# Kernel optimization log

Hardware: AMD Instinct MI355X
Metric: run time of the kernel (lower is better)

The kernel has to match this reference:

```python
import jax, jax.numpy as jnp
import numpy as np

B, S, V, D, H, KVH, L = 2, 1024, 8192, 1024, 16, 4, 8
HD = D // H          # 64, head dim
KV = KVH * HD        # 256, kv projection width
HID = 2736           # max(16, ceil(2*4*1024/48)*16)
NS = 4               # num_skip_weights = min(L//2, L - L//2)
SOFTCAP = 30.0
ROPE_BASE = 10000.0
RS_INIT = 1.0 / np.sqrt(L)


def setup_inputs() -> dict:
    key = jax.random.key(0)
    ks = iter(jax.random.split(key, 64))
    def rn(shape, s=0.02):
        return jax.random.normal(next(ks), shape, dtype=jnp.float32) * s
    inp = {}
    inp['idx'] = jax.random.randint(next(ks), (B, S), 0, V)
    inp['tok_emb'] = rn((V, D))
    inp['embed_norm_w'] = 1.0 + rn((D,))
    inp['resid_mix'] = jnp.stack([1.0 + rn((L, D), 0.05), rn((L, D), 0.05)], axis=1)  # [L,2,D]
    inp['attn_norm_w'] = 1.0 + rn((L, D))
    inp['mlp_norm_w'] = 1.0 + rn((L, D))
    inp['attn_scale'] = RS_INIT + rn((L, D))
    inp['mlp_scale'] = RS_INIT + rn((L, D))
    inp['Wq'] = rn((L, D, D))
    inp['Wk'] = rn((L, KV, D))
    inp['Wv'] = rn((L, KV, D))
    conv = lambda C: rn((L, 3, C), 0.1).at[:, 2, :].add(1.0)  # curr ~ 1, prev ~ 0
    inp['q_conv_w'] = conv(D)
    inp['k_conv_w'] = conv(KV)
    inp['v_conv_w'] = conv(KV)
    inp['q_gain'] = jnp.eye(H, dtype=jnp.float32)[None] + rn((L, H, H))
    inp['post_attn_norm_w'] = 1.0 + rn((L, D))
    inp['Wo'] = rn((L, D, D))
    inp['Wfc'] = rn((L, HID, D))
    inp['Wgate'] = rn((L, HID, D))
    inp['h_conv_w'] = rn((L, 3, HID), 0.1).at[:, 2, :].add(1.0)
    inp['h_norm_w'] = 1.0 + rn((L, HID))
    inp['Wmproj'] = rn((L, D, HID))
    inp['skip_weights'] = RS_INIT + rn((NS, D))
    inp['skip_gates'] = rn((NS, D), 0.1)
    inp['final_norm_w'] = 1.0 + rn((D,))
    inp['lm_head_w'] = rn((V, D))
    inp['bigram_head'] = rn((V, V))
    inp['bigram_scale'] = 0.02 + rn((V,), 0.005)
    inp['bigram_gate'] = rn((D,), 0.1)
    inp['unigram_bias'] = rn((V,), 0.01)
    return inp


def _rmsnorm(x, w=None):
    eps = jnp.finfo(x.dtype).eps
    y = x * jax.lax.rsqrt(jnp.mean(x * x, axis=-1, keepdims=True) + eps)
    return y * w if w is not None else y


def _dwconv(x, w):  # x [B,S,C], w [3,C]: causal depthwise 3-tap conv
    n = x.shape[1]
    xp = jnp.pad(x, ((0, 0), (2, 0), (0, 0)))
    return w[0] * xp[:, :n] + w[1] * xp[:, 1:n + 1] + w[2] * xp[:, 2:]


def _rope_tables(seqlen):
    inv_freq = 1.0 / (ROPE_BASE ** (jnp.arange(0, HD, 2, dtype=jnp.float32) / HD))
    freqs = jnp.outer(jnp.arange(seqlen, dtype=jnp.float32), inv_freq)  # [S, HD//2]
    return jnp.cos(freqs)[None, None], jnp.sin(freqs)[None, None]


def _apply_rope(x, cos, sin):
    half = x.shape[-1] // 2
    x1, x2 = x[..., :half], x[..., half:]
    return jnp.concatenate([x1 * cos + x2 * sin, -x1 * sin + x2 * cos], axis=-1)


def reference(idx, tok_emb, embed_norm_w, resid_mix, attn_norm_w, mlp_norm_w, attn_scale, mlp_scale, Wq, Wk, Wv, q_conv_w, k_conv_w, v_conv_w, q_gain, post_attn_norm_w, Wo, Wfc, Wgate, h_conv_w, h_norm_w, Wmproj, skip_weights, skip_gates, final_norm_w, lm_head_w, bigram_head, bigram_scale, bigram_gate, unigram_bias):
    cos, sin = _rope_tables(S)
    causal = jnp.tril(jnp.ones((S, S), dtype=bool))

    def attn(x, i):
        q = _dwconv(x @ Wq[i].T, q_conv_w[i]).reshape(B, S, H, HD).transpose(0, 2, 1, 3)
        k = _dwconv(x @ Wk[i].T, k_conv_w[i]).reshape(B, S, KVH, HD).transpose(0, 2, 1, 3)
        v = _dwconv(x @ Wv[i].T, v_conv_w[i]).reshape(B, S, KVH, HD).transpose(0, 2, 1, 3)
        q = _apply_rope(_rmsnorm(q), cos, sin)
        k = _apply_rope(_rmsnorm(k), cos, sin)
        q = jnp.einsum('hg,bgsd->bhsd', q_gain[i], q)
        kr = jnp.repeat(k, H // KVH, axis=1)
        vr = jnp.repeat(v, H // KVH, axis=1)
        scores = jnp.einsum('bhsd,bhtd->bhst', q, kr) / np.sqrt(HD).astype(np.float32)
        scores = jnp.where(causal, scores, -jnp.inf)
        p = jax.nn.softmax(scores, axis=-1)
        y = jnp.einsum('bhst,bhtd->bhsd', p, vr).transpose(0, 2, 1, 3).reshape(B, S, D)
        return _rmsnorm(y, post_attn_norm_w[i]) @ Wo[i].T

    def mlp(x, i):
        h = (x @ Wfc[i].T) * jax.nn.silu(x @ Wgate[i].T)
        h = _rmsnorm(_dwconv(h, h_conv_w[i]), h_norm_w[i])
        return h @ Wmproj[i].T

    def block(x, x0, i):
        x = resid_mix[i, 0] * x + resid_mix[i, 1] * x0
        x = x + attn_scale[i] * attn(_rmsnorm(x, attn_norm_w[i]), i)
        x = x + mlp_scale[i] * mlp(_rmsnorm(x, mlp_norm_w[i]), i)
        return x

    x = _rmsnorm(tok_emb[idx], embed_norm_w)
    x0 = x
    enc = L // 2
    skips = []
    for i in range(enc):
        x = block(x, x0, i)
        skips.append(x)
    for j in range(L - enc):
        if j < NS:
            x = x + (skip_weights[j] * jax.nn.sigmoid(skip_gates[j]))[None, None, :] * skips.pop()
        x = block(x, x0, enc + j)
    x = _rmsnorm(x, final_norm_w)

    logits = x @ lm_head_w.T + unigram_bias
    gate = jax.nn.sigmoid(x @ bigram_gate)[..., None]        # [B,S,1]
    logits = logits + gate * (bigram_head[idx] * bigram_scale)
    return SOFTCAP * jnp.tanh(logits / SOFTCAP)
```

## Files before the change

### kernel.cpp

```cpp
#include <hip/hip_runtime.h>
#include <hip/hip_bf16.h>
#include <cstdint>
#include <cstddef>

#define B_   2
#define S_   1024
#define V_   8192
#define D_   1024
#define H_   16
#define KVH_ 4
#define L_   8
#define HD_  64
#define KV_  256
#define HID_ 2736
#define HIDP 2752
#define NT_  (B_*S_)
#define EPSF 1.1920928955078125e-7f
#define SOFTCAPF 30.0f

typedef __bf16 bf8 __attribute__((ext_vector_type(8)));
typedef __bf16 bf4 __attribute__((ext_vector_type(4)));
typedef float  f4  __attribute__((ext_vector_type(4)));

#define GLDS16(g, l) __builtin_amdgcn_global_load_lds( \
    (const __attribute__((address_space(1))) void*)(g), \
    (__attribute__((address_space(3))) void*)(l), 16, 0, 0)

__device__ __forceinline__ float wsum(float v){
#pragma unroll
  for (int m = 32; m >= 1; m >>= 1) v += __shfl_xor(v, m, 64);
  return v;
}
__device__ __forceinline__ float blocksum256(float v){
  __shared__ float red[4];
  v = wsum(v);
  if ((threadIdx.x & 63) == 0) red[threadIdx.x >> 6] = v;
  __syncthreads();
  return red[0] + red[1] + red[2] + red[3];
}
__device__ __forceinline__ float4 ld4b(const __bf16* p, size_t i4){
  bf4 v = ((const bf4*)p)[i4];
  return make_float4((float)v[0], (float)v[1], (float)v[2], (float)v[3]);
}

template<int BM, int BN, int OUT>
__global__ __launch_bounds__(256) void k_gemm(
    const __bf16* __restrict__ A, const __bf16* __restrict__ Wt,
    void* __restrict__ Cv, int M, int N, int K, int lda, int mtiles)
{
  constexpr int SMEM = (BM + BN) * 128;
  __shared__ __attribute__((aligned(16))) unsigned char smem[SMEM];
  __bf16* As = (__bf16*)smem;
  __bf16* Bs = (__bf16*)(smem + BM*128);

  const int tid  = threadIdx.x;
  const int nwg = gridDim.x;
  const int wg  = (blockIdx.x & 7) * (nwg >> 3) + (blockIdx.x >> 3);
  const int bm   = wg % mtiles;
  const int bn   = wg / mtiles;
  const int m0   = bm * BM, n0 = bn * BN;
  const int lane = tid & 63, wv = tid >> 6;
  const int wm   = (wv >> 1) * (BM / 2);
  const int wn   = (wv & 1) * (BN / 2);
  const int fr   = lane & 15, g = lane >> 4;
  constexpr int MI = BM / 32;
  constexpr int NJ = BN / 32;
  constexpr int AP = BM / 32;
  constexpr int BP = BN / 32;

  f4 acc[MI][NJ] = {};

  const int rs = lane >> 3, ss = lane & 7;
  const int cseg = ss ^ ((wv*8 + rs) & 7);
  const __bf16* aq[AP];
#pragma unroll
  for (int p = 0; p < AP; ++p)
    aq[p] = A + (size_t)(m0 + wv*8 + p*32 + rs) * lda + cseg*8;
  const __bf16* bq[BP];
#pragma unroll
  for (int p = 0; p < BP; ++p) {
    int rB = n0 + wv*8 + p*32 + rs; if (rB > N-1) rB = N-1;
    bq[p] = Wt + (size_t)rB * K + cseg*8;
  }

  for (int k0 = 0; k0 < K; k0 += 64) {
    __syncthreads();
#pragma unroll
    for (int p = 0; p < AP; ++p) GLDS16(aq[p] + k0, As + (wv*8 + p*32)*64);
#pragma unroll
    for (int p = 0; p < BP; ++p) GLDS16(bq[p] + k0, Bs + (wv*8 + p*32)*64);
    __syncthreads();

#pragma unroll
    for (int ks = 0; ks < 2; ++ks) {
      const int sgo = (((ks*4 + g) ^ (fr & 7)) << 3);
      bf8 af[MI], bf[NJ];
#pragma unroll
      for (int i = 0; i < MI; ++i)
        af[i] = *(const bf8*)&As[(wm + i*16 + fr)*64 + sgo];
#pragma unroll
      for (int j = 0; j < NJ; ++j)
        bf[j] = *(const bf8*)&Bs[(wn + j*16 + fr)*64 + sgo];
#pragma unroll
      for (int i = 0; i < MI; ++i)
#pragma unroll
        for (int j = 0; j < NJ; ++j)
          acc[i][j] = __builtin_amdgcn_mfma_f32_16x16x32_bf16(af[i], bf[j], acc[i][j], 0, 0, 0);
    }
  }

  const int rbase = g << 2;
#pragma unroll
  for (int i = 0; i < MI; ++i) {
    int gm = m0 + wm + i*16 + rbase;
#pragma unroll
    for (int j = 0; j < NJ; ++j) {
      int gn = n0 + wn + j*16 + fr;
      if (gn < N) {
        if constexpr (OUT == 1) {
#pragma unroll
          for (int r = 0; r < 4; ++r)
            ((__bf16*)Cv)[(size_t)(gm + r) * N + gn] = (__bf16)acc[i][j][r];
        } else {
#pragma unroll
          for (int r = 0; r < 4; ++r)
            ((float*)Cv)[(size_t)(gm + r) * N + gn] = acc[i][j][r];
        }
      }
    }
  }
}

#define STG8(t, h, b) do { \
    if ((h) < 2) { \
      const __bf16* _s = A + (size_t)(m0 + (h)*128 + w16 + rsub) * lda + (t)*32 + sseg*8; \
      GLDS16(_s, smem + (b)*32768 + ((h)*128 + w16) * 64); \
    } else { \
      int _rB = n0 + ((h)-2)*128 + w16 + rsub; if (_rB > N-1) _rB = N-1; \
      const __bf16* _s = Wt + (size_t)_rB * K + (t)*32 + sseg*8; \
      GLDS16(_s, smem + (b)*32768 + 16384 + (((h)-2)*128 + w16) * 64); \
    } } while (0)

#define LDA8(b, r, gg) (*(const bf8*)(smem + (b)*32768 + (r)*64 + (((gg) ^ ((((r)>>3)&1)<<1)))*16))
#define LDB8(b, r, gg) (*(const bf8*)(smem + (b)*32768 + 16384 + (r)*64 + (((gg) ^ ((((r)>>3)&1)<<1)))*16))

#define PH8(bt, q, dostage, st, sh, sb, W) do { \
    const int _r0 = wr*128 + ((q)>>1)*64 + fr; \
    const int _c0 = wc*64 + ((q)&1)*32 + fr; \
    bf8 _a0 = LDA8(bt, _r0 +  0, g); \
    bf8 _a1 = LDA8(bt, _r0 + 16, g); \
    bf8 _a2 = LDA8(bt, _r0 + 32, g); \
    bf8 _a3 = LDA8(bt, _r0 + 48, g); \
    bf8 _b0 = LDB8(bt, _c0 +  0, g); \
    bf8 _b1 = LDB8(bt, _c0 + 16, g); \
    if (dostage) STG8(st, sh, sb); \
    if ((W) == 4)      asm volatile("s_waitcnt vmcnt(4)" ::: "memory"); \
    else if ((W) == 0) asm volatile("s_waitcnt vmcnt(0)" ::: "memory"); \
    asm volatile("" ::: "memory"); \
    __builtin_amdgcn_s_barrier(); \
    asm volatile("" ::: "memory"); \
    __builtin_amdgcn_s_setprio(1); \
    acc[((q)>>1)*4+0][((q)&1)*2+0] = __builtin_amdgcn_mfma_f32_16x16x32_bf16(_a0, _b0, acc[((q)>>1)*4+0][((q)&1)*2+0], 0,0,0); \
    acc[((q)>>1)*4+0][((q)&1)*2+1] = __builtin_amdgcn_mfma_f32_16x16x32_bf16(_a0, _b1, acc[((q)>>1)*4+0][((q)&1)*2+1], 0,0,0); \
    acc[((q)>>1)*4+1][((q)&1)*2+0] = __builtin_amdgcn_mfma_f32_16x16x32_bf16(_a1, _b0, acc[((q)>>1)*4+1][((q)&1)*2+0], 0,0,0); \
    acc[((q)>>1)*4+1][((q)&1)*2+1] = __builtin_amdgcn_mfma_f32_16x16x32_bf16(_a1, _b1, acc[((q)>>1)*4+1][((q)&1)*2+1], 0,0,0); \
    acc[((q)>>1)*4+2][((q)&1)*2+0] = __builtin_amdgcn_mfma_f32_16x16x32_bf16(_a2, _b0, acc[((q)>>1)*4+2][((q)&1)*2+0], 0,0,0); \
    acc[((q)>>1)*4+2][((q)&1)*2+1] = __builtin_amdgcn_mfma_f32_16x16x32_bf16(_a2, _b1, acc[((q)>>1)*4+2][((q)&1)*2+1], 0,0,0); \
    acc[((q)>>1)*4+3][((q)&1)*2+0] = __builtin_amdgcn_mfma_f32_16x16x32_bf16(_a3, _b0, acc[((q)>>1)*4+3][((q)&1)*2+0], 0,0,0); \
    acc[((q)>>1)*4+3][((q)&1)*2+1] = __builtin_amdgcn_mfma_f32_16x16x32_bf16(_a3, _b1, acc[((q)>>1)*4+3][((q)&1)*2+1], 0,0,0); \
    __builtin_amdgcn_s_setprio(0); \
    asm volatile("" ::: "memory"); \
    __builtin_amdgcn_s_barrier(); \
    asm volatile("" ::: "memory"); \
  } while (0)

template<int OUT>
__global__ __launch_bounds__(512, 2) void k_gemm8(
    const __bf16* __restrict__ A, const __bf16* __restrict__ Wt,
    void* __restrict__ Cv, int M, int N, int K, int lda, int mtiles,
    const int* __restrict__ idx, const float* __restrict__ gateb,
    const float* __restrict__ bhd, const float* __restrict__ bsc,
    const float* __restrict__ ub)
{
  __shared__ __attribute__((aligned(16))) unsigned char smem[98304];
  const int tid = threadIdx.x;
  const int nwg = gridDim.x;
  const int wg  = (blockIdx.x & 7) * (nwg >> 3) + (blockIdx.x >> 3);
  const int bm = wg % mtiles, bnn = wg / mtiles;
  const int m0 = bm << 8, n0 = bnn << 8;
  const int l = tid & 63, wid = tid >> 6;
  const int wr = wid >> 2, wc = wid & 3;
  const int fr = l & 15, g = l >> 4;

  f4 acc[8][4] = {};

  const int w16  = wid * 16;
  const int rsub = l >> 2;
  const int sseg = (l & 3) ^ ((l >= 32) ? 2 : 0);

  const int nk = K >> 5;
  const int ni = nk >> 1;

  STG8(0, 0, 0); STG8(0, 1, 0); STG8(0, 2, 0); STG8(0, 3, 0);
  STG8(1, 0, 1); STG8(1, 1, 1); STG8(1, 2, 1); STG8(1, 3, 1);
  asm volatile("s_waitcnt vmcnt(4)" ::: "memory");
  asm volatile("" ::: "memory");
  __builtin_amdgcn_s_barrier();
  asm volatile("" ::: "memory");

  int b0 = 0;
  for (int i = 0; i < ni; ++i) {
    const int b1 = (b0 == 2) ? 0 : b0 + 1;
    const int b2 = (b1 == 2) ? 0 : b1 + 1;
    const bool nlast = (i + 1 < ni);
    const int t2 = 2*i + 2, t3 = 2*i + 3;
    PH8(b0, 0, nlast, t2, 0, b2, -1);
    PH8(b0, 1, nlast, t2, 1, b2, -1);
    PH8(b0, 2, nlast, t2, 2, b2, -1);
    PH8(b0, 3, nlast, t2, 3, b2, nlast ? 4 : 0);
    PH8(b1, 0, nlast, t3, 0, b0, -1);
    PH8(b1, 1, nlast, t3, 1, b0, -1);
    PH8(b1, 2, nlast, t3, 2, b0, -1);
    PH8(b1, 3, nlast, t3, 3, b0, nlast ? 4 : -1);
    b0 = b2;
  }

  if constexpr (OUT == 1) {
    __bf16* C = (__bf16*)Cv;
#pragma unroll
    for (int ii = 0; ii < 8; ++ii) {
      int gm = m0 + wr*128 + ii*16 + g*4;
#pragma unroll
      for (int j = 0; j < 4; ++j) {
        int gn = n0 + wc*64 + j*16 + fr;
        if (gn < N) {
#pragma unroll
          for (int r = 0; r < 4; ++r)
            C[(size_t)(gm + r) * N + gn] = (__bf16)acc[ii][j][r];
        }
      }
    }
  } else {
    float* EP = (float*)smem;
    __syncthreads();
#pragma unroll
    for (int pass = 0; pass < 4; ++pass) {
      if (wr == (pass >> 1)) {
#pragma unroll
        for (int a = 0; a < 4; ++a) {
          int ii = (pass & 1)*4 + a;
#pragma unroll
          for (int j = 0; j < 4; ++j)
#pragma unroll
            for (int r = 0; r < 4; ++r)
              EP[(a*16 + g*4 + r)*256 + wc*64 + j*16 + fr] = acc[ii][j][r];
        }
      }
      __syncthreads();
#pragma unroll
      for (int it = 0; it < 8; ++it) {
        int row = it*8 + (tid >> 6);
        int c0  = (tid & 63) << 2;
        int grow = m0 + pass*64 + row;
        int gn = n0 + c0;
        float gt = gateb[grow];
        int tk = idx[grow];
        float4 a4 = *(float4*)&EP[row*256 + c0];
        float4 b4 = *(const float4*)&bhd[(size_t)tk * V_ + gn];
        float4 u4 = *(const float4*)&ub[gn];
        float4 s4 = *(const float4*)&bsc[gn];
        float4 o;
        o.x = SOFTCAPF * tanhf((a4.x + u4.x + gt*b4.x*s4.x) / SOFTCAPF);
        o.y = SOFTCAPF * tanhf((a4.y + u4.y + gt*b4.y*s4.y) / SOFTCAPF);
        o.z = SOFTCAPF * tanhf((a4.z + u4.z + gt*b4.z*s4.z) / SOFTCAPF);
        o.w = SOFTCAPF * tanhf((a4.w + u4.w + gt*b4.w*s4.w) / SOFTCAPF);
        *(float4*)&((float*)Cv)[(size_t)grow * N + gn] = o;
      }
      __syncthreads();
    }
  }
}
#undef PH8
#undef LDA8
#undef LDB8
#undef STG8

__global__ void k_cvt(const float* __restrict__ s, __bf16* __restrict__ d,
                      int perL, int K, int Kpad, long dstL, long dstOff, long nd4)
{
  long i = (long)blockIdx.x * 256 + threadIdx.x;
  if (i >= nd4) return;
  const int kp4 = Kpad >> 2;
  long row = i / kp4;
  int  c   = (int)(i % kp4) << 2;
  long layer = row / perL, r = row % perL;
  bf4 o;
  if (c < K) {
    float4 v = *(const float4*)(s + (layer*perL + r) * (long)K + c);
    o[0] = (__bf16)v.x; o[1] = (__bf16)v.y; o[2] = (__bf16)v.z; o[3] = (__bf16)v.w;
  } else { o[0] = o[1] = o[2] = o[3] = (__bf16)0.f; }
  *(bf4*)(d + layer*dstL + dstOff + (long)r*Kpad + c) = o;
}

__global__ void k_embed(const int* __restrict__ idx, const float* __restrict__ emb,
                        const float* __restrict__ wn, float* __restrict__ x, float* __restrict__ x0)
{
  const int r = blockIdx.x, t = threadIdx.x;
  const float4 v = ((const float4*)(emb + (size_t)idx[r] * D_))[t];
  float ss = blocksum256(v.x*v.x + v.y*v.y + v.z*v.z + v.w*v.w);
  float rs = rsqrtf(ss / (float)D_ + EPSF);
  const float4 w = ((const float4*)wn)[t];
  float4 o = make_float4(v.x*rs*w.x, v.y*rs*w.y, v.z*rs*w.z, v.w*rs*w.w);
  ((float4*)(x  + (size_t)r * D_))[t] = o;
  ((float4*)(x0 + (size_t)r * D_))[t] = o;
}

__global__ void k_blockstart(
    float* __restrict__ x, const float* __restrict__ x0,
    const __bf16* __restrict__ t1, const float* __restrict__ msc,
    float* __restrict__ skstore, const float* __restrict__ skread, int same,
    const float* __restrict__ skw, const float* __restrict__ skg,
    const float* __restrict__ mix, const float* __restrict__ nw,
    __bf16* __restrict__ xn)
{
  const int r = blockIdx.x, t = threadIdx.x;
  const size_t i4 = (size_t)r * 256 + t;
  float4 xv = ((float4*)x)[i4];
  if (t1) {
    float4 tv = ld4b(t1, i4);
    float4 s  = ((const float4*)msc)[t];
    xv.x += s.x*tv.x; xv.y += s.y*tv.y; xv.z += s.z*tv.z; xv.w += s.w*tv.w;
  }
  if (skstore) ((float4*)skstore)[i4] = xv;
  if (skw) {
    float4 sv;
    if (same) sv = xv;
    else      sv = ((const float4*)skread)[i4];
    float4 w = ((const float4*)skw)[t];
    float4 g = ((const float4*)skg)[t];
    xv.x += w.x / (1.f + __expf(-g.x)) * sv.x;
    xv.y += w.y / (1.f + __expf(-g.y)) * sv.y;
    xv.z += w.z / (1.f + __expf(-g.z)) * sv.z;
    xv.w += w.w / (1.f + __expf(-g.w)) * sv.w;
  }
  float4 x0v = ((const float4*)x0)[i4];
  float4 m0  = ((const float4*)mix)[t];
  float4 m1  = ((const float4*)(mix + D_))[t];
  float4 nv;
  nv.x = m0.x*xv.x + m1.x*x0v.x; nv.y = m0.y*xv.y + m1.y*x0v.y;
  nv.z = m0.z*xv.z + m1.z*x0v.z; nv.w = m0.w*xv.w + m1.w*x0v.w;
  ((float4*)x)[i4] = nv;
  float ss = blocksum256(nv.x*nv.x + nv.y*nv.y + nv.z*nv.z + nv.w*nv.w);
  float rs = rsqrtf(ss / (float)D_ + EPSF);
  const float4 w = ((const float4*)nw)[t];
  bf4 o = { (__bf16)(nv.x*rs*w.x), (__bf16)(nv.y*rs*w.y),
            (__bf16)(nv.z*rs*w.z), (__bf16)(nv.w*rs*w.w) };
  ((bf4*)xn)[i4] = o;
}

__global__ void k_addnorm(float* __restrict__ x, const __bf16* __restrict__ t1,
                          const float* __restrict__ sc, const float* __restrict__ nw,
                          __bf16* __restrict__ xn,
                          const float* __restrict__ bg, float* __restrict__ gateb)
{
  const int r = blockIdx.x, t = threadIdx.x;
  const size_t i4 = (size_t)r * 256 + t;
  float4 xv = ((float4*)x)[i4];
  float4 tv = ld4b(t1, i4);
  float4 s  = ((const float4*)sc)[t];
  xv.x += s.x*tv.x; xv.y += s.y*tv.y; xv.z += s.z*tv.z; xv.w += s.w*tv.w;
  ((float4*)x)[i4] = xv;
  float ss = blocksum256(xv.x*xv.x + xv.y*xv.y + xv.z*xv.z + xv.w*xv.w);
  float rs = rsqrtf(ss / (float)D_ + EPSF);
  const float4 w = ((const float4*)nw)[t];
  float ox = xv.x*rs*w.x, oy = xv.y*rs*w.y, oz = xv.z*rs*w.z, ow = xv.w*rs*w.w;
  bf4 o = { (__bf16)ox, (__bf16)oy, (__bf16)oz, (__bf16)ow };
  ((bf4*)xn)[i4] = o;
  if (bg) {
    float4 b4 = ((const float4*)bg)[t];
    float gd = ox*b4.x + oy*b4.y + oz*b4.z + ow*b4.w;
    __syncthreads();
    float gs = blocksum256(gd);
    if (t == 0) gateb[r] = 1.f / (1.f + __expf(-gs));
  }
}

__global__ void k_rmsnormb(const float* __restrict__ in, const float* __restrict__ w,
                           __bf16* __restrict__ out)
{
  const int r = blockIdx.x, t = threadIdx.x;
  float4 v = ((const float4*)(in + (size_t)r * D_))[t];
  float ss = blocksum256(v.x*v.x + v.y*v.y + v.z*v.z + v.w*v.w);
  float rs = rsqrtf(ss / (float)D_ + EPSF);
  const float4 w4 = ((const float4*)w)[t];
  bf4 o = { (__bf16)(v.x*rs*w4.x), (__bf16)(v.y*rs*w4.y),
            (__bf16)(v.z*rs*w4.z), (__bf16)(v.w*rs*w4.w) };
  ((bf4*)(out + (size_t)r * D_))[t] = o;
}

__device__ __forceinline__ float conv3b(const __bf16* buf, int tok, int s, int ld, int col,
                                        const float* w, int C, int c){
  const __bf16* p0 = buf + (size_t)tok * ld + col;
  float a  = (s >= 2) ? (float)p0[-2*ld] : 0.f;
  float bb = (s >= 1) ? (float)p0[-ld]   : 0.f;
  return w[c]*a + w[C + c]*bb + w[2*C + c]*(float)p0[0];
}

__global__ __launch_bounds__(256) void k_prep(
    const __bf16* __restrict__ qkv,
    const float* __restrict__ qcw, const float* __restrict__ kcw, const float* __restrict__ vcw,
    const float* __restrict__ qgain,
    __bf16* __restrict__ q2, __bf16* __restrict__ k2, __bf16* __restrict__ v2)
{
  const int tok = blockIdx.x;
  const int s = tok & (S_ - 1);
  const int t = threadIdx.x, lane = t & 63, w = t >> 6;
  __shared__ float qsh[1024];

  const int j = lane & 31;
  float freq = __expf(-(float)j * (9.210340371976184f / 32.f));
  float sn, cs;
  __sincosf((float)s * freq, &sn, &cs);

#pragma unroll
  for (int k = 0; k < 4; ++k) {
    int c = t + k*256;
    float qc = conv3b(qkv, tok, s, 1536, c, qcw, D_, c);
    float ssq = wsum(qc * qc);
    float qn = qc * rsqrtf(ssq / 64.f + EPSF);
    float pr = __shfl_xor(qn, 32, 64);
    qsh[c] = qn * cs + ((lane < 32) ? pr * sn : -pr * sn);
  }
  __syncthreads();
  float qg[16];
#pragma unroll
  for (int g = 0; g < 16; ++g) qg[g] = qsh[g*64 + lane];
#pragma unroll
  for (int k = 0; k < 4; ++k) {
    int h = (k << 2) + w;
    float acc = 0.f;
#pragma unroll
    for (int g = 0; g < 16; ++g) acc += qgain[h*16 + g] * qg[g];
    q2[(size_t)tok * D_ + h*64 + lane] = (__bf16)acc;
  }

  {
    float kc = conv3b(qkv, tok, s, 1536, 1024 + t, kcw, KV_, t);
    float ssk = wsum(kc * kc);
    float kn = kc * rsqrtf(ssk / 64.f + EPSF);
    float pk = __shfl_xor(kn, 32, 64);
    k2[(size_t)tok * KV_ + t] = (__bf16)(kn * cs + ((lane < 32) ? pk * sn : -pk * sn));
  }
  v2[(size_t)tok * KV_ + t] = (__bf16)conv3b(qkv, tok, s, 1536, 1280 + t, vcw, KV_, t);
}

#define LDK 72
__global__ __launch_bounds__(256) void k_attn(
    const __bf16* __restrict__ q2, const __bf16* __restrict__ k2,
    const __bf16* __restrict__ v2, float* __restrict__ y)
{
  __shared__ __attribute__((aligned(16))) __bf16 Ks[64*LDK];
  __shared__ __attribute__((aligned(16))) __bf16 Vt[64*LDK];
  __shared__ __attribute__((aligned(16))) __bf16 Ps[4][16*LDK];

  const int id = blockIdx.x;
  const int h  = (id >> 4) & 15;
  const int b  = id >> 8;
  const int qb = b ? (15 - (id & 15)) : (id & 15);
  const int tid = threadIdx.x, l = tid & 63, wq = tid >> 6;
  const int g = l >> 4, fr = l & 15;
  const int kvh = h >> 2;
  const int qrow = qb*64 + wq*16 + fr;

  bf8 qf[2];
#pragma unroll
  for (int ks = 0; ks < 2; ++ks)
    qf[ks] = *(const bf8*)&q2[(size_t)(b*S_ + qrow)*D_ + h*64 + g*8 + ks*32];

  float m = -1e30f, lsum = 0.f;
  f4 acc[4] = {};

  const int nch = qb + 1;
  for (int ch = 0; ch < nch; ++ch) {
    const int t0 = ch << 6;
    __syncthreads();
#pragma unroll
    for (int it = 0; it < 2; ++it) {
      int i = tid + it*256;
      int row = i >> 3, seg = (i & 7) << 3;
      *(bf8*)&Ks[row*LDK + seg] =
        *(const bf8*)&k2[(size_t)(b*S_ + t0 + row)*KV_ + kvh*64 + seg];
    }
    {
      int key4 = (tid & 15) << 2, hd4 = (tid >> 4) << 2;
      bf4 vv[4];
#pragma unroll
      for (int kk = 0; kk < 4; ++kk)
        vv[kk] = *(const bf4*)&v2[(size_t)(b*S_ + t0 + key4 + kk)*KV_ + kvh*64 + hd4];
#pragma unroll
      for (int hh = 0; hh < 4; ++hh) {
        bf4 w = { vv[0][hh], vv[1][hh], vv[2][hh], vv[3][hh] };
        *(bf4*)&Vt[(hd4 + hh)*LDK + key4] = w;
      }
    }
    __syncthreads();

    f4 sc[4] = {};
#pragma unroll
    for (int ks = 0; ks < 2; ++ks)
#pragma unroll
      for (int t = 0; t < 4; ++t) {
        bf8 kf = *(const bf8*)&Ks[(t*16 + fr)*LDK + g*8 + ks*32];
        sc[t] = __builtin_amdgcn_mfma_f32_16x16x32_bf16(kf, qf[ks], sc[t], 0, 0, 0);
      }

    const bool lastch = (ch == qb);
    float s[4][4];
    float pmax = -1e30f;
#pragma unroll
    for (int t = 0; t < 4; ++t)
#pragma unroll
      for (int r = 0; r < 4; ++r) {
        float v = sc[t][r] * 0.125f;
        if (lastch && (t0 + t*16 + g*4 + r > qrow)) v = -1e30f;
        s[t][r] = v;
        pmax = fmaxf(pmax, v);
      }
    pmax = fmaxf(pmax, __shfl_xor(pmax, 16, 64));
    pmax = fmaxf(pmax, __shfl_xor(pmax, 32, 64));
    float mnew = fmaxf(m, pmax);
    float alpha = __expf(m - mnew);
    float rs = 0.f;
#pragma unroll
    for (int t = 0; t < 4; ++t)
#pragma unroll
      for (int r = 0; r < 4; ++r) { float p = __expf(s[t][r] - mnew); s[t][r] = p; rs += p; }
    rs += __shfl_xor(rs, 16, 64);
    rs += __shfl_xor(rs, 32, 64);
    lsum = lsum * alpha + rs;
    m = mnew;
#pragma unroll
    for (int t = 0; t < 4; ++t) acc[t] = acc[t] * alpha;

#pragma unroll
    for (int t = 0; t < 4; ++t) {
      bf4 pw = { (__bf16)s[t][0], (__bf16)s[t][1], (__bf16)s[t][2], (__bf16)s[t][3] };
      *(bf4*)&Ps[wq][fr*LDK + t*16 + g*4] = pw;
    }

#pragma unroll
    for (int ks = 0; ks < 2; ++ks) {
      bf8 pf = *(const bf8*)&Ps[wq][fr*LDK + g*8 + ks*32];
#pragma unroll
      for (int t = 0; t < 4; ++t) {
        bf8 vf = *(const bf8*)&Vt[(t*16 + fr)*LDK + g*8 + ks*32];
        acc[t] = __builtin_amdgcn_mfma_f32_16x16x32_bf16(vf, pf, acc[t], 0, 0, 0);
      }
    }
  }

  float inv = 1.f / lsum;
#pragma unroll
  for (int t = 0; t < 4; ++t)
#pragma unroll
    for (int r = 0; r < 4; ++r)
      y[(size_t)(b*S_ + qrow)*D_ + h*64 + t*16 + g*4 + r] = acc[t][r] * inv;
}

__device__ __forceinline__ float hprodb(const __bf16* row, int c){
  float a = (float)row[c], b = (float)row[HID_ + c];
  return a * b / (1.f + __expf(-b));
}
__global__ __launch_bounds__(256) void k_hfuse(
    const __bf16* __restrict__ hb, const float* __restrict__ cw,
    const float* __restrict__ nw, __bf16* __restrict__ out)
{
  const int tok = blockIdx.x, t = threadIdx.x;
  const int s = tok & (S_ - 1);
  const __bf16* row0 = hb + (size_t)tok * 5472;
  float v[11]; float ss = 0.f;
#pragma unroll
  for (int ii = 0; ii < 11; ++ii) {
    int c = t + ii*256;
    float cv = 0.f;
    if (c < HID_) {
      float p0 = hprodb(row0, c);
      float p1 = (s >= 1) ? hprodb(row0 - 5472, c) : 0.f;
      float p2 = (s >= 2) ? hprodb(row0 - 2*5472, c) : 0.f;
      cv = cw[c]*p2 + cw[HID_ + c]*p1 + cw[2*HID_ + c]*p0;
    }
    v[ii] = cv; ss += cv*cv;
  }
  ss = blocksum256(ss);
  float rs = rsqrtf(ss / (float)HID_ + EPSF);
#pragma unroll
  for (int ii = 0; ii < 11; ++ii) {
    int c = t + ii*256;
    if (c < HIDP)
      out[(size_t)tok * HIDP + c] = (c < HID_) ? (__bf16)(v[ii]*rs*nw[c]) : (__bf16)0.f;
  }
}

template<int BM, int BN, int OUT>
static inline void gemm(const __bf16* A, const __bf16* W, void* C, int M, int N, int K,
                        int lda, hipStream_t s)
{
  int mt = M / BM, nt = (N + BN - 1) / BN;
  k_gemm<BM, BN, OUT><<<dim3(mt * nt), dim3(256), 0, s>>>(A, W, C, M, N, K, lda, mt);
}

template<int OUT>
static inline void gemm8(const __bf16* A, const __bf16* W, void* C, int M, int N, int K,
                         int lda, hipStream_t s,
                         const int* idx = nullptr, const float* gateb = nullptr,
                         const float* bhd = nullptr, const float* bsc = nullptr,
                         const float* ub = nullptr)
{
  int mt = M >> 8, nt = (N + 255) >> 8;
  k_gemm8<OUT><<<dim3(mt * nt), dim3(512), 0, s>>>(A, W, C, M, N, K, lda, mt,
                                                   idx, gateb, bhd, bsc, ub);
}

extern "C" void kernel_launch(void* const* d_in, const int* in_sizes, int n_in,
                              void* d_out, int out_size, void* d_ws, size_t ws_size,
                              hipStream_t stream)
{
  const int*   idx    = (const int*)d_in[0];
  const float* temb   = (const float*)d_in[1];
  const float* enw    = (const float*)d_in[2];
  const float* rmix   = (const float*)d_in[3];
  const float* anw    = (const float*)d_in[4];
  const float* mnw    = (const float*)d_in[5];
  const float* ascale = (const float*)d_in[6];
  const float* mscale = (const float*)d_in[7];
  const float* Wq     = (const float*)d_in[8];
  const float* Wk     = (const float*)d_in[9];
  const float* Wv     = (const float*)d_in[10];
  const float* qcw    = (const float*)d_in[11];
  const float* kcw    = (const float*)d_in[12];
  const float* vcw    = (const float*)d_in[13];
  const float* qgain  = (const float*)d_in[14];
  const float* panw   = (const float*)d_in[15];
  const float* Wo     = (const float*)d_in[16];
  const float* Wfc    = (const float*)d_in[17];
  const float* Wgate  = (const float*)d_in[18];
  const float* hcw    = (const float*)d_in[19];
  const float* hnw    = (const float*)d_in[20];
  const float* Wmp    = (const float*)d_in[21];
  const float* skw    = (const float*)d_in[22];
  const float* skg    = (const float*)d_in[23];
  const float* fnw    = (const float*)d_in[24];
  const float* lmw    = (const float*)d_in[25];
  const float* bh     = (const float*)d_in[26];
  const float* bsc    = (const float*)d_in[27];
  const float* bg     = (const float*)d_in[28];
  const float* ub     = (const float*)d_in[29];

  float* p = (float*)d_ws;
  float* x    = p; p += (size_t)NT_ * D_;
  float* x0   = p; p += (size_t)NT_ * D_;
  float* y    = p; p += (size_t)NT_ * D_;
  float* skips= p; p += (size_t)4 * NT_ * D_;
  float* gateb= p; p += NT_;
  __bf16* qkvb= (__bf16*)p; p += (size_t)NT_ * 1536 / 2;
  __bf16* hbb = (__bf16*)p; p += (size_t)NT_ * 5472 / 2;
  __bf16* t1b = (__bf16*)p; p += (size_t)NT_ * D_ / 2;
  __bf16* xnb = (__bf16*)p; p += (size_t)NT_ * D_ / 2;
  __bf16* q2b = (__bf16*)p; p += (size_t)NT_ * D_ / 2;
  __bf16* k2b = (__bf16*)p; p += (size_t)NT_ * KV_ / 2;
  __bf16* v2b = (__bf16*)p; p += (size_t)NT_ * KV_ / 2;
  __bf16* hnb = (__bf16*)p; p += (size_t)NT_ * HIDP / 2;
  __bf16* wqkv= (__bf16*)p; p += (size_t)L_ * 1536 * 1024 / 2;
  __bf16* wob = (__bf16*)p; p += (size_t)L_ * 1024 * 1024 / 2;
  __bf16* wfcg= (__bf16*)p; p += (size_t)L_ * 5472 * 1024 / 2;
  __bf16* wmpb= (__bf16*)p; p += (size_t)L_ * 1024 * HIDP / 2;
  __bf16* wlmb= (__bf16*)p; p += (size_t)V_ * 1024 / 2;
  float* logits = (float*)d_out;

  auto cvt = [&](const float* s, __bf16* d, int perL, int K, int Kpad,
                 long dstL, long dstOff, int nl) {
    long nd4 = (long)nl * perL * (Kpad >> 2);
    int grid = (int)((nd4 + 255) / 256);
    k_cvt<<<grid, 256, 0, stream>>>(s, d, perL, K, Kpad, dstL, dstOff, nd4);
  };
  cvt(Wq,    wqkv, 1024, 1024, 1024, 1536L*1024, 0,          L_);
  cvt(Wk,    wqkv,  256, 1024, 1024, 1536L*1024, 1024L*1024, L_);
  cvt(Wv,    wqkv,  256, 1024, 1024, 1536L*1024, 1280L*1024, L_);
  cvt(Wo,    wob,  1024, 1024, 1024, 1024L*1024, 0,          L_);
  cvt(Wfc,   wfcg, 2736, 1024, 1024, 5472L*1024, 0,          L_);
  cvt(Wgate, wfcg, 2736, 1024, 1024, 5472L*1024, 2736L*1024, L_);
  cvt(Wmp,   wmpb, 1024, 2736, HIDP, 1024L*HIDP, 0,          L_);
  cvt(lmw,   wlmb, 8192, 1024, 1024, 8192L*1024, 0,          1);

  k_embed<<<NT_, 256, 0, stream>>>(idx, temb, enw, x, x0);

  for (int i = 0; i < L_; ++i) {
    const float* pmsc = (i > 0) ? mscale + (size_t)(i-1) * D_ : nullptr;
    float* skst = (i >= 1 && i <= 4) ? skips + (size_t)(i-1) * NT_ * D_ : nullptr;
    const float* skrd = (i >= 4) ? skips + (size_t)(7-i) * NT_ * D_ : nullptr;
    const float* swp = (i >= 4) ? skw + (size_t)(i-4) * D_ : nullptr;
    const float* sgp = (i >= 4) ? skg + (size_t)(i-4) * D_ : nullptr;
    k_blockstart<<<NT_, 256, 0, stream>>>(x, x0, (i > 0) ? t1b : nullptr, pmsc,
                                          skst, skrd, (i == 4) ? 1 : 0, swp, sgp,
                                          rmix + (size_t)i * 2 * D_,
                                          anw + (size_t)i * D_, xnb);
    gemm<64, 128, 1>(xnb, wqkv + (size_t)i * 1536 * 1024, qkvb, NT_, 1536, 1024, 1024, stream);
    k_prep<<<NT_, 256, 0, stream>>>(qkvb,
                                    qcw + (size_t)i * 3 * D_, kcw + (size_t)i * 3 * KV_,
                                    vcw + (size_t)i * 3 * KV_, qgain + (size_t)i * H_ * H_,
                                    q2b, k2b, v2b);
    k_attn<<<B_ * H_ * (S_/64), 256, 0, stream>>>(q2b, k2b, v2b, y);
    k_rmsnormb<<<NT_, 256, 0, stream>>>(y, panw + (size_t)i * D_, xnb);
    gemm<64, 64, 1>(xnb, wob + (size_t)i * 1024 * 1024, t1b, NT_, 1024, 1024, 1024, stream);
    k_addnorm<<<NT_, 256, 0, stream>>>(x, t1b, ascale + (size_t)i * D_,
                                       mnw + (size_t)i * D_, xnb, nullptr, nullptr);
    gemm8<1>(xnb, wfcg + (size_t)i * 5472 * 1024, hbb, NT_, 5472, 1024, 1024, stream);
    k_hfuse<<<NT_, 256, 0, stream>>>(hbb, hcw + (size_t)i * 3 * HID_,
                                     hnw + (size_t)i * HID_, hnb);
    gemm<64, 64, 1>(hnb, wmpb + (size_t)i * 1024 * HIDP, t1b, NT_, 1024, HIDP, HIDP, stream);
  }

  k_addnorm<<<NT_, 256, 0, stream>>>(x, t1b, mscale + (size_t)7 * D_, fnw, xnb, bg, gateb);
  gemm8<2>(xnb, wlmb, logits, NT_, V_, 1024, 1024, stream, idx, gateb, bh, bsc, ub);
}
```

Measured before the change: 1.906 ms.

## Split-K the per-layer GEMMs and sum bf16 partials in consumer kernels

The QKV, Wo, FC/gate and mproj GEMMs now use split-K (4, 4, 2 and 4 ways). Each K slice writes its own bf16 partial buffer, and the downstream elementwise kernels (prep conv, hfuse, blockstart, addnorm) sum the partials when they read. This raises the workgroup count so the small GEMMs fill more CUs, but it adds partial-buffer traffic and rounds each partial to bf16 before the sum. The FC GEMM also moves from the 256x256 gemm8 kernel to the simpler 64x128 kernel, and HIDP is padded to 2816 so K divides evenly by the split.

```diff
diff --git a/kernel.cpp b/kernel.cpp
--- a/kernel.cpp
+++ b/kernel.cpp
@@ -13,7 +13,7 @@
 #define HD_  64
 #define KV_  256
 #define HID_ 2736
-#define HIDP 2752
+#define HIDP 2816
 #define NT_  (B_*S_)
 #define EPSF 1.1920928955078125e-7f
 #define SOFTCAPF 30.0f
@@ -43,7 +43,7 @@
   return make_float4((float)v[0], (float)v[1], (float)v[2], (float)v[3]);
 }
 
-template<int BM, int BN, int OUT>
+template<int BM, int BN, int SK>
 __global__ __launch_bounds__(256) void k_gemm(
     const __bf16* __restrict__ A, const __bf16* __restrict__ Wt,
     void* __restrict__ Cv, int M, int N, int K, int lda, int mtiles)
@@ -56,9 +56,13 @@
   const int tid  = threadIdx.x;
   const int nwg = gridDim.x;
   const int wg  = (blockIdx.x & 7) * (nwg >> 3) + (blockIdx.x >> 3);
-  const int bm   = wg % mtiles;
-  const int bn   = wg / mtiles;
+  const int kz   = (SK > 1) ? (wg % SK) : 0;
+  const int wgt  = (SK > 1) ? (wg / SK) : wg;
+  const int bm   = wgt % mtiles;
+  const int bn   = wgt / mtiles;
   const int m0   = bm * BM, n0 = bn * BN;
+  const int Keff = K / SK;
+  const int koff = kz * Keff;
   const int lane = tid & 63, wv = tid >> 6;
   const int wm   = (wv >> 1) * (BM / 2);
   const int wn   = (wv & 1) * (BN / 2);
@@ -75,15 +79,15 @@
   const __bf16* aq[AP];
 #pragma unroll
   for (int p = 0; p < AP; ++p)
-    aq[p] = A + (size_t)(m0 + wv*8 + p*32 + rs) * lda + cseg*8;
+    aq[p] = A + (size_t)(m0 + wv*8 + p*32 + rs) * lda + koff + cseg*8;
   const __bf16* bq[BP];
 #pragma unroll
   for (int p = 0; p < BP; ++p) {
     int rB = n0 + wv*8 + p*32 + rs; if (rB > N-1) rB = N-1;
-    bq[p] = Wt + (size_t)rB * K + cseg*8;
-  }
-
-  for (int k0 = 0; k0 < K; k0 += 64) {
+    bq[p] = Wt + (size_t)rB * K + koff + cseg*8;
+  }
+
+  for (int k0 = 0; k0 < Keff; k0 += 64) {
     __syncthreads();
 #pragma unroll
     for (int p = 0; p < AP; ++p) GLDS16(aq[p] + k0, As + (wv*8 + p*32)*64);
@@ -110,6 +114,7 @@
   }
 
   const int rbase = g << 2;
+  __bf16* Cb = (__bf16*)Cv + (size_t)kz * M * N;
 #pragma unroll
   for (int i = 0; i < MI; ++i) {
     int gm = m0 + wm + i*16 + rbase;
@@ -117,15 +122,9 @@
     for (int j = 0; j < NJ; ++j) {
       int gn = n0 + wn + j*16 + fr;
       if (gn < N) {
-        if constexpr (OUT == 1) {
-#pragma unroll
-          for (int r = 0; r < 4; ++r)
-            ((__bf16*)Cv)[(size_t)(gm + r) * N + gn] = (__bf16)acc[i][j][r];
-        } else {
-#pragma unroll
-          for (int r = 0; r < 4; ++r)
-            ((float*)Cv)[(size_t)(gm + r) * N + gn] = acc[i][j][r];
-        }
+#pragma unroll
+        for (int r = 0; r < 4; ++r)
+          Cb[(size_t)(gm + r) * N + gn] = (__bf16)acc[i][j][r];
       }
     }
   }
@@ -174,7 +173,6 @@
     asm volatile("" ::: "memory"); \
   } while (0)
 
-template<int OUT>
 __global__ __launch_bounds__(512, 2) void k_gemm8(
     const __bf16* __restrict__ A, const __bf16* __restrict__ Wt,
     void* __restrict__ Cv, int M, int N, int K, int lda, int mtiles,
@@ -225,59 +223,42 @@
     b0 = b2;
   }
 
-  if constexpr (OUT == 1) {
-    __bf16* C = (__bf16*)Cv;
-#pragma unroll
-    for (int ii = 0; ii < 8; ++ii) {
-      int gm = m0 + wr*128 + ii*16 + g*4;
-#pragma unroll
-      for (int j = 0; j < 4; ++j) {
-        int gn = n0 + wc*64 + j*16 + fr;
-        if (gn < N) {
+  float* EP = (float*)smem;
+  __syncthreads();
+#pragma unroll
+  for (int pass = 0; pass < 4; ++pass) {
+    if (wr == (pass >> 1)) {
+#pragma unroll
+      for (int a = 0; a < 4; ++a) {
+        int ii = (pass & 1)*4 + a;
+#pragma unroll
+        for (int j = 0; j < 4; ++j)
 #pragma unroll
           for (int r = 0; r < 4; ++r)
-            C[(size_t)(gm + r) * N + gn] = (__bf16)acc[ii][j][r];
-        }
+            EP[(a*16 + g*4 + r)*256 + wc*64 + j*16 + fr] = acc[ii][j][r];
       }
     }
-  } else {
-    float* EP = (float*)smem;
     __syncthreads();
 #pragma unroll
-    for (int pass = 0; pass < 4; ++pass) {
-      if (wr == (pass >> 1)) {
-#pragma unroll
-        for (int a = 0; a < 4; ++a) {
-          int ii = (pass & 1)*4 + a;
-#pragma unroll
-          for (int j = 0; j < 4; ++j)
-#pragma unroll
-            for (int r = 0; r < 4; ++r)
-              EP[(a*16 + g*4 + r)*256 + wc*64 + j*16 + fr] = acc[ii][j][r];
-        }
-      }
-      __syncthreads();
-#pragma unroll
-      for (int it = 0; it < 8; ++it) {
-        int row = it*8 + (tid >> 6);
-        int c0  = (tid & 63) << 2;
-        int grow = m0 + pass*64 + row;
-        int gn = n0 + c0;
-        float gt = gateb[grow];
-        int tk = idx[grow];
-        float4 a4 = *(float4*)&EP[row*256 + c0];
-        float4 b4 = *(const float4*)&bhd[(size_t)tk * V_ + gn];
-        float4 u4 = *(const float4*)&ub[gn];
-        float4 s4 = *(const float4*)&bsc[gn];
-        float4 o;
-        o.x = SOFTCAPF * tanhf((a4.x + u4.x + gt*b4.x*s4.x) / SOFTCAPF);
-        o.y = SOFTCAPF * tanhf((a4.y + u4.y + gt*b4.y*s4.y) / SOFTCAPF);
-        o.z = SOFTCAPF * tanhf((a4.z + u4.z + gt*b4.z*s4.z) / SOFTCAPF);
-        o.w = SOFTCAPF * tanhf((a4.w + u4.w + gt*b4.w*s4.w) / SOFTCAPF);
-        *(float4*)&((float*)Cv)[(size_t)grow * N + gn] = o;
-      }
-      __syncthreads();
-    }
+    for (int it = 0; it < 8; ++it) {
+      int row = it*8 + (tid >> 6);
+      int c0  = (tid & 63) << 2;
+      int grow = m0 + pass*64 + row;
+      int gn = n0 + c0;
+      float gt = gateb[grow];
+      int tk = idx[grow];
+      float4 a4 = *(float4*)&EP[row*256 + c0];
+      float4 b4 = *(const float4*)&bhd[(size_t)tk * V_ + gn];
+      float4 u4 = *(const float4*)&ub[gn];
+      float4 s4 = *(const float4*)&bsc[gn];
+      float4 o;
+      o.x = SOFTCAPF * tanhf((a4.x + u4.x + gt*b4.x*s4.x) / SOFTCAPF);
+      o.y = SOFTCAPF * tanhf((a4.y + u4.y + gt*b4.y*s4.y) / SOFTCAPF);
+      o.z = SOFTCAPF * tanhf((a4.z + u4.z + gt*b4.z*s4.z) / SOFTCAPF);
+      o.w = SOFTCAPF * tanhf((a4.w + u4.w + gt*b4.w*s4.w) / SOFTCAPF);
+      *(float4*)&((float*)Cv)[(size_t)grow * N + gn] = o;
+    }
+    __syncthreads();
   }
 }
 #undef PH8
@@ -315,6 +296,14 @@
   ((float4*)(x0 + (size_t)r * D_))[t] = o;
 }
 
+__device__ __forceinline__ float4 sum4p(const __bf16* t1, size_t i4){
+  float4 a = ld4b(t1, i4);
+  float4 b = ld4b(t1 + (size_t)NT_ * D_, i4);
+  float4 c = ld4b(t1 + (size_t)2 * NT_ * D_, i4);
+  float4 d = ld4b(t1 + (size_t)3 * NT_ * D_, i4);
+  return make_float4(a.x+b.x+c.x+d.x, a.y+b.y+c.y+d.y, a.z+b.z+c.z+d.z, a.w+b.w+c.w+d.w);
+}
+
 __global__ void k_blockstart(
     float* __restrict__ x, const float* __restrict__ x0,
     const __bf16* __restrict__ t1, const float* __restrict__ msc,
@@ -327,7 +316,7 @@
   const size_t i4 = (size_t)r * 256 + t;
   float4 xv = ((float4*)x)[i4];
   if (t1) {
-    float4 tv = ld4b(t1, i4);
+    float4 tv = sum4p(t1, i4);
     float4 s  = ((const float4*)msc)[t];
     xv.x += s.x*tv.x; xv.y += s.y*tv.y; xv.z += s.z*tv.z; xv.w += s.w*tv.w;
   }
@@ -366,7 +355,7 @@
   const int r = blockIdx.x, t = threadIdx.x;
   const size_t i4 = (size_t)r * 256 + t;
   float4 xv = ((float4*)x)[i4];
-  float4 tv = ld4b(t1, i4);
+  float4 tv = sum4p(t1, i4);
   float4 s  = ((const float4*)sc)[t];
   xv.x += s.x*tv.x; xv.y += s.y*tv.y; xv.z += s.z*tv.z; xv.w += s.w*tv.w;
   ((float4*)x)[i4] = xv;
@@ -398,12 +387,17 @@
   ((bf4*)(out + (size_t)r * D_))[t] = o;
 }
 
-__device__ __forceinline__ float conv3b(const __bf16* buf, int tok, int s, int ld, int col,
-                                        const float* w, int C, int c){
-  const __bf16* p0 = buf + (size_t)tok * ld + col;
-  float a  = (s >= 2) ? (float)p0[-2*ld] : 0.f;
-  float bb = (s >= 1) ? (float)p0[-ld]   : 0.f;
-  return w[c]*a + w[C + c]*bb + w[2*C + c]*(float)p0[0];
+__device__ __forceinline__ float conv3b4(const __bf16* b0, int tok, int s, int ld, int col,
+                                         const float* w, int C, int c, size_t pstr){
+  float a = 0.f, bb = 0.f, cc = 0.f;
+#pragma unroll
+  for (int p = 0; p < 4; ++p) {
+    const __bf16* pp = b0 + p*pstr + (size_t)tok * ld + col;
+    if (s >= 2) a  += (float)pp[-2*ld];
+    if (s >= 1) bb += (float)pp[-ld];
+    cc += (float)pp[0];
+  }
+  return w[c]*a + w[C + c]*bb + w[2*C + c]*cc;
 }
 
 __global__ __launch_bounds__(256) void k_prep(
@@ -416,6 +410,7 @@
   const int s = tok & (S_ - 1);
   const int t = threadIdx.x, lane = t & 63, w = t >> 6;
   __shared__ float qsh[1024];
+  const size_t PSTR = (size_t)NT_ * 1536;
 
   const int j = lane & 31;
   float freq = __expf(-(float)j * (9.210340371976184f / 32.f));
@@ -425,7 +420,7 @@
 #pragma unroll
   for (int k = 0; k < 4; ++k) {
     int c = t + k*256;
-    float qc = conv3b(qkv, tok, s, 1536, c, qcw, D_, c);
+    float qc = conv3b4(qkv, tok, s, 1536, c, qcw, D_, c, PSTR);
     float ssq = wsum(qc * qc);
     float qn = qc * rsqrtf(ssq / 64.f + EPSF);
     float pr = __shfl_xor(qn, 32, 64);
@@ -445,13 +440,13 @@
   }
 
   {
-    float kc = conv3b(qkv, tok, s, 1536, 1024 + t, kcw, KV_, t);
+    float kc = conv3b4(qkv, tok, s, 1536, 1024 + t, kcw, KV_, t, PSTR);
     float ssk = wsum(kc * kc);
     float kn = kc * rsqrtf(ssk / 64.f + EPSF);
     float pk = __shfl_xor(kn, 32, 64);
     k2[(size_t)tok * KV_ + t] = (__bf16)(kn * cs + ((lane < 32) ? pk * sn : -pk * sn));
   }
-  v2[(size_t)tok * KV_ + t] = (__bf16)conv3b(qkv, tok, s, 1536, 1280 + t, vcw, KV_, t);
+  v2[(size_t)tok * KV_ + t] = (__bf16)conv3b4(qkv, tok, s, 1536, 1280 + t, vcw, KV_, t, PSTR);
 }
 
 #define LDK 72
@@ -567,8 +562,9 @@
       y[(size_t)(b*S_ + qrow)*D_ + h*64 + t*16 + g*4 + r] = acc[t][r] * inv;
 }
 
-__device__ __forceinline__ float hprodb(const __bf16* row, int c){
-  float a = (float)row[c], b = (float)row[HID_ + c];
+__device__ __forceinline__ float hprodb2(const __bf16* r0, const __bf16* r1, int c){
+  float a = (float)r0[c] + (float)r1[c];
+  float b = (float)r0[HID_ + c] + (float)r1[HID_ + c];
   return a * b / (1.f + __expf(-b));
 }
 __global__ __launch_bounds__(256) void k_hfuse(
@@ -578,15 +574,16 @@
   const int tok = blockIdx.x, t = threadIdx.x;
   const int s = tok & (S_ - 1);
   const __bf16* row0 = hb + (size_t)tok * 5472;
+  const __bf16* row1 = row0 + (size_t)NT_ * 5472;
   float v[11]; float ss = 0.f;
 #pragma unroll
   for (int ii = 0; ii < 11; ++ii) {
     int c = t + ii*256;
     float cv = 0.f;
     if (c < HID_) {
-      float p0 = hprodb(row0, c);
-      float p1 = (s >= 1) ? hprodb(row0 - 5472, c) : 0.f;
-      float p2 = (s >= 2) ? hprodb(row0 - 2*5472, c) : 0.f;
+      float p0 = hprodb2(row0, row1, c);
+      float p1 = (s >= 1) ? hprodb2(row0 - 5472, row1 - 5472, c) : 0.f;
+      float p2 = (s >= 2) ? hprodb2(row0 - 2*5472, row1 - 2*5472, c) : 0.f;
       cv = cw[c]*p2 + cw[HID_ + c]*p1 + cw[2*HID_ + c]*p0;
     }
     v[ii] = cv; ss += cv*cv;
@@ -601,24 +598,12 @@
   }
 }
 
-template<int BM, int BN, int OUT>
+template<int BM, int BN, int SK>
 static inline void gemm(const __bf16* A, const __bf16* W, void* C, int M, int N, int K,
                         int lda, hipStream_t s)
 {
   int mt = M / BM, nt = (N + BN - 1) / BN;
-  k_gemm<BM, BN, OUT><<<dim3(mt * nt), dim3(256), 0, s>>>(A, W, C, M, N, K, lda, mt);
-}
-
-template<int OUT>
-static inline void gemm8(const __bf16* A, const __bf16* W, void* C, int M, int N, int K,
-                         int lda, hipStream_t s,
-                         const int* idx = nullptr, const float* gateb = nullptr,
-                         const float* bhd = nullptr, const float* bsc = nullptr,
-                         const float* ub = nullptr)
-{
-  int mt = M >> 8, nt = (N + 255) >> 8;
-  k_gemm8<OUT><<<dim3(mt * nt), dim3(512), 0, s>>>(A, W, C, M, N, K, lda, mt,
-                                                   idx, gateb, bhd, bsc, ub);
+  k_gemm<BM, BN, SK><<<dim3(mt * nt * SK), dim3(256), 0, s>>>(A, W, C, M, N, K, lda, mt);
 }
 
 extern "C" void kernel_launch(void* const* d_in, const int* in_sizes, int n_in,
@@ -662,9 +647,9 @@
   float* y    = p; p += (size_t)NT_ * D_;
   float* skips= p; p += (size_t)4 * NT_ * D_;
   float* gateb= p; p += NT_;
-  __bf16* qkvb= (__bf16*)p; p += (size_t)NT_ * 1536 / 2;
-  __bf16* hbb = (__bf16*)p; p += (size_t)NT_ * 5472 / 2;
-  __bf16* t1b = (__bf16*)p; p += (size_t)NT_ * D_ / 2;
+  __bf16* qkvb= (__bf16*)p; p += (size_t)4 * NT_ * 1536 / 2;
+  __bf16* hbb = (__bf16*)p; p += (size_t)2 * NT_ * 5472 / 2;
+  __bf16* t1b = (__bf16*)p; p += (size_t)4 * NT_ * D_ / 2;
   __bf16* xnb = (__bf16*)p; p += (size_t)NT_ * D_ / 2;
   __bf16* q2b = (__bf16*)p; p += (size_t)NT_ * D_ / 2;
   __bf16* k2b = (__bf16*)p; p += (size_t)NT_ * KV_ / 2;
@@ -704,22 +689,26 @@
                                           skst, skrd, (i == 4) ? 1 : 0, swp, sgp,
                                           rmix + (size_t)i * 2 * D_,
                                           anw + (size_t)i * D_, xnb);
-    gemm<64, 128, 1>(xnb, wqkv + (size_t)i * 1536 * 1024, qkvb, NT_, 1536, 1024, 1024, stream);
+    gemm<64, 128, 4>(xnb, wqkv + (size_t)i * 1536 * 1024, qkvb, NT_, 1536, 1024, 1024, stream);
     k_prep<<<NT_, 256, 0, stream>>>(qkvb,
                                     qcw + (size_t)i * 3 * D_, kcw + (size_t)i * 3 * KV_,
                                     vcw + (size_t)i * 3 * KV_, qgain + (size_t)i * H_ * H_,
                                     q2b, k2b, v2b);
     k_attn<<<B_ * H_ * (S_/64), 256, 0, stream>>>(q2b, k2b, v2b, y);
     k_rmsnormb<<<NT_, 256, 0, stream>>>(y, panw + (size_t)i * D_, xnb);
-    gemm<64, 64, 1>(xnb, wob + (size_t)i * 1024 * 1024, t1b, NT_, 1024, 1024, 1024, stream);
+    gemm<64, 64, 4>(xnb, wob + (size_t)i * 1024 * 1024, t1b, NT_, 1024, 1024, 1024, stream);
     k_addnorm<<<NT_, 256, 0, stream>>>(x, t1b, ascale + (size_t)i * D_,
                                        mnw + (size_t)i * D_, xnb, nullptr, nullptr);
-    gemm8<1>(xnb, wfcg + (size_t)i * 5472 * 1024, hbb, NT_, 5472, 1024, 1024, stream);
+    gemm<64, 128, 2>(xnb, wfcg + (size_t)i * 5472 * 1024, hbb, NT_, 5472, 1024, 1024, stream);
     k_hfuse<<<NT_, 256, 0, stream>>>(hbb, hcw + (size_t)i * 3 * HID_,
                                      hnw + (size_t)i * HID_, hnb);
-    gemm<64, 64, 1>(hnb, wmpb + (size_t)i * 1024 * HIDP, t1b, NT_, 1024, HIDP, HIDP, stream);
+    gemm<64, 64, 4>(hnb, wmpb + (size_t)i * 1024 * HIDP, t1b, NT_, 1024, HIDP, HIDP, stream);
   }
 
   k_addnorm<<<NT_, 256, 0, stream>>>(x, t1b, mscale + (size_t)7 * D_, fnw, xnb, bg, gateb);
-  gemm8<2>(xnb, wlmb, logits, NT_, V_, 1024, 1024, stream, idx, gateb, bh, bsc, ub);
-}
+  {
+    int mt = NT_ >> 8, nt = V_ >> 8;
+    k_gemm8<<<dim3(mt * nt), dim3(512), 0, stream>>>(xnb, wlmb, logits, NT_, V_, 1024, 1024, mt,
+                                                     idx, gateb, bh, bsc, ub);
+  }
+}
```

Result: no change. 1.896 ms (-0.5%).
